# Performance work log

Hardware: AMD Instinct MI355X
Metric: run time of the kernel (lower is better)

The kernel has to match this reference:

```python
import jax, jax.numpy as jnp
import numpy as np

EPS = 1e-12

def _pdist(a, b):
    # a: [B,N,3], b: [B,M,3] -> [B,N,M] L2 distances (no huge [B,N,M,3] temp)
    sq = (jnp.sum(a * a, -1)[:, :, None] + jnp.sum(b * b, -1)[:, None, :]
          - 2.0 * jnp.einsum('bnd,bmd->bnm', a, b))
    return jnp.sqrt(jnp.maximum(sq, EPS))

def _loss_terms(skel_xyz, skel_radius, skel_nori, l3_xyz, shape_all):
    normal = shape_all[:, :, 3:6]
    shape_xyz = shape_all[:, :, :3]
    B, Ns, _ = skel_xyz.shape
    N = shape_xyz.shape[1]

    # --- loss_sample: 8 surface samples per sphere ---
    e = 0.57735027
    dirs = jnp.array([[e, e, e], [e, e, -e], [e, -e, e], [e, -e, -e],
                      [-e, e, e], [-e, e, -e], [-e, -e, e], [-e, -e, -e]],
                     dtype=skel_xyz.dtype)
    centers = jnp.repeat(skel_xyz, 8, axis=1)
    radii = jnp.repeat(skel_radius, 8, axis=1)
    sample_xyz = centers + radii * jnp.tile(dirs, (Ns, 1))[None]

    d_ss = _pdist(shape_xyz, sample_xyz)
    cd1 = jnp.sum(jnp.min(d_ss, axis=1)) / (Ns * 8)    # sample -> shape
    cd2 = jnp.sum(jnp.min(d_ss, axis=2)) / N           # shape -> sample
    loss_sample = cd1 + cd2

    # --- point2sphere / sphere2point ---
    d_sc = _pdist(shape_xyz, skel_xyz)                 # [B, N, Ns]
    sph = jnp.abs(d_sc - skel_radius[:, None, :, 0])
    loss_p2s = jnp.sum(jnp.min(sph, axis=2)) / N + jnp.sum(jnp.min(sph, axis=1)) / Ns

    loss_radius = -jnp.sum(skel_radius) / Ns

    # --- loss_normal: 30-NN of skel in shape, |dot(nori, shape normal)| ---
    d_ks = _pdist(skel_xyz, shape_xyz)                 # [B, Ns, N]
    idx30 = jax.lax.top_k(-d_ks, 30)[1]                # [B, Ns, 30]
    nn_nrm = jnp.take_along_axis(normal[:, None, :, :], idx30[..., None], axis=2)
    dots = jnp.einsum('bjd,bjkd->bjk', skel_nori, nn_nrm)
    loss_normal = jnp.sum(jnp.mean(jnp.abs(dots), axis=2)) / B

    # --- loss_skelenormal: points swept along nori, vs l3_xyz ---
    ks = (jnp.arange(30, dtype=skel_xyz.dtype) / 30.0)[None, :, None, None]
    combine = (skel_xyz[:, None] + skel_nori[:, None] * ks).reshape(B, 30 * Ns, 3)
    mind = jnp.min(_pdist(combine, l3_xyz), axis=2)
    loss_skn = 50.0 * jnp.sum(mind) / (B * Ns * 30)
    loss_skn = loss_skn + 500.0 * jnp.sum(jnp.var(mind, axis=1, ddof=1)) / B

    # --- loss_normaldist: exp barrier + hard penalty on |nori| ---
    nrm = jnp.sqrt(jnp.sum(skel_nori * skel_nori, -1) + EPS)
    loss_nd = jnp.sum(jnp.exp(-(nrm - 0.3)) + jnp.where(nrm < 0.25, 5.0, 0.0)) / (B * Ns)

    # --- loss_normalsmooth: 3-NN (incl. self) nori consistency ---
    idx3 = jax.lax.top_k(-_pdist(skel_xyz, skel_xyz), 3)[1]   # [B, Ns, 3]
    nn_nori = jnp.take_along_axis(skel_nori[:, None, :, :], idx3[..., None], axis=2)
    diff = skel_nori[:, :, None, :] - nn_nori
    loss_ns = jnp.sum(jnp.sqrt(jnp.sum(diff * diff, -1) + EPS)) / (B * Ns * 3)

    return loss_sample, loss_p2s, loss_radius, loss_normal, loss_skn, loss_nd, loss_ns

def setup_inputs() -> dict:
    key = jax.random.key(0)
    ks = jax.random.split(key, 9)
    B, N, Ns, M = 8, 4096, 256, 256
    return {
        'skel_xyz': jax.random.normal(ks[0], (B, Ns, 3), jnp.float32),
        'skel_radius': jax.random.uniform(ks[1], (B, Ns, 1), jnp.float32),
        'shape_cmb_features': jax.random.normal(ks[2], (B, Ns, 32), jnp.float32),
        'skel_nori': jax.random.normal(ks[3], (B, Ns, 3), jnp.float32),
        'weights': jax.random.uniform(ks[4], (B, Ns, 8), jnp.float32),
        'l3_xyz': jax.random.normal(ks[5], (B, M, 3), jnp.float32),
        'l3_normals': jax.random.normal(ks[6], (B, M, 3), jnp.float32),
        'shape_xyz': jax.random.normal(ks[7], (B, N, 6), jnp.float32),
        'A': jax.random.uniform(ks[8], (B, Ns, Ns), jnp.float32),
        'w0': 1, 'w1': 1, 'w2': 1, 'w3': 1, 'w4': 1, 'w5': 1, 'w6': 1,
    }

def reference(skel_xyz, skel_radius, shape_cmb_features, skel_nori, weights,
              l3_xyz, l3_normals, shape_xyz, A,
              w0, w1, w2, w3, w4, w5, w6):
    ls, lp, lr, ln, lskn, lnd, lns = _loss_terms(
        skel_xyz, skel_radius, skel_nori, l3_xyz, shape_xyz)
    # lap_reg=False -> loss_smooth = 0 (w3 term vanishes)
    return (w0 * ls + lp * w1 + lr * w2 + ln * w4 + lskn * w5
            + w6 * lnd + 0.1 * lns)
```

## Files before the change

### kernel.cpp

```cpp
#include <hip/hip_runtime.h>
#include <math.h>

#define EPS 1e-12f
#define EDIR 0.57735027f
#define M2E  -1.15470054f

#define NB 8
#define NS 256
#define NP 4096
#define NM 256

#define NBLK_SKEL 2048
#define NBLK_CD1  2048
#define NBLK_CD2  4096
#define NBLK_SKN  960
#define B0_CD1  (NBLK_SKEL)
#define B0_CD2  (B0_CD1 + NBLK_CD1)
#define B0_SKN  (B0_CD2 + NBLK_CD2)
#define NBLK_MEGA (B0_SKN + NBLK_SKN)

#define OFF_SKO 0
#define OFF_C1O (OFF_SKO + 2048*4)
#define OFF_C2O (OFF_C1O + 2048)
#define OFF_P2O (OFF_C2O + 4096)
#define OFF_SKS (OFF_P2O + 4096)
#define OFF_SKQ (OFF_SKS + 960)

__device__ __forceinline__ unsigned umin2(unsigned a, unsigned b){ return a<b?a:b; }
__device__ __forceinline__ unsigned umax2(unsigned a, unsigned b){ return a>b?a:b; }

__device__ __forceinline__ float wave_min(float v){
#pragma unroll
  for (int o = 32; o; o >>= 1) v = fminf(v, __shfl_xor(v, o));
  return v;
}
__device__ __forceinline__ float wave_max(float v){
#pragma unroll
  for (int o = 32; o; o >>= 1) v = fmaxf(v, __shfl_xor(v, o));
  return v;
}
__device__ __forceinline__ float wave_sum(float v){
#pragma unroll
  for (int o = 32; o; o >>= 1) v += __shfl_xor(v, o);
  return v;
}
__device__ __forceinline__ unsigned wave_min_u(unsigned v){
#pragma unroll
  for (int o = 32; o; o >>= 1){ unsigned w = __shfl_xor(v, o); v = (w < v) ? w : v; }
  return v;
}
__device__ __forceinline__ unsigned wave_max_u(unsigned v){
#pragma unroll
  for (int o = 32; o; o >>= 1){ unsigned w = __shfl_xor(v, o); v = (w > v) ? w : v; }
  return v;
}
__device__ __forceinline__ unsigned long long wave_min_u64(unsigned long long v){
#pragma unroll
  for (int o = 32; o; o >>= 1){
    unsigned long long w = __shfl_xor(v, o);
    v = (w < v) ? w : v;
  }
  return v;
}

__global__ __launch_bounds__(64) void k_mega(const float* __restrict__ skel,
                                             const float* __restrict__ rad,
                                             const float* __restrict__ nori,
                                             const float* __restrict__ l3,
                                             const float* __restrict__ shape,
                                             float* __restrict__ ws){
  __shared__ float4 lsh[NM];
  int bid  = blockIdx.x;
  int lane = threadIdx.x;

  if (bid < B0_CD1){
    int row = bid;
    int b = row >> 8;
    const float* sjp = skel + (size_t)row * 3;
    float cx = sjp[0], cy = sjp[1], cz = sjp[2];
    float rj = rad[row];
    float r2j = rj * rj;
    const float* njp = nori + (size_t)row * 3;
    float nx = njp[0], ny = njp[1], nz = njp[2];
    const float* shb = shape + (size_t)b * NP * 6;

    unsigned a0=~0u,a1=~0u,a2=~0u,a3=~0u,a4=~0u,a5=~0u;
    unsigned b0=~0u,b1=~0u,b2=~0u,b3=~0u,b4=~0u,b5=~0u;
    float dmoA = 3.4e38f, dmiA = -3.4e38f, dmoB = 3.4e38f, dmiB = -3.4e38f;

#pragma unroll 2
    for (int s = 0; s < 32; ++s){
      int nA = s * 128 + lane;
      int nB = nA + 64;
      float2 xyA = *(const float2*)(shb + (size_t)nA * 6);
      float  zA  = shb[(size_t)nA * 6 + 2];
      float2 xyB = *(const float2*)(shb + (size_t)nB * 6);
      float  zB  = shb[(size_t)nB * 6 + 2];
      float dxA = xyA.x - cx, dyA = xyA.y - cy, dzA = zA - cz;
      float dxB = xyB.x - cx, dyB = xyB.y - cy, dzB = zB - cz;
      float dA = fmaf(dxA, dxA, fmaf(dyA, dyA, dzA * dzA));
      float dB = fmaf(dxB, dxB, fmaf(dyB, dyB, dzB * dzB));
      bool inA = dA < r2j;
      bool inB = dB < r2j;
      dmoA = fminf(dmoA, inA ? 3.4e38f : dA);
      dmiA = fmaxf(dmiA, inA ? dA : -3.4e38f);
      dmoB = fminf(dmoB, inB ? 3.4e38f : dB);
      dmiB = fmaxf(dmiB, inB ? dB : -3.4e38f);
      unsigned uA = (__float_as_uint(dA) & 0xFFFFF000u) | (unsigned)nA;
      unsigned uB = (__float_as_uint(dB) & 0xFFFFF000u) | (unsigned)nB;
      a5 = umin2(a5, uA);
      { unsigned p = umin2(a4, a5), q = umax2(a4, a5); a4 = p; a5 = q; }
      { unsigned p = umin2(a3, a4), q = umax2(a3, a4); a3 = p; a4 = q; }
      { unsigned p = umin2(a2, a3), q = umax2(a2, a3); a2 = p; a3 = q; }
      { unsigned p = umin2(a1, a2), q = umax2(a1, a2); a1 = p; a2 = q; }
      { unsigned p = umin2(a0, a1), q = umax2(a0, a1); a0 = p; a1 = q; }
      b5 = umin2(b5, uB);
      { unsigned p = umin2(b4, b5), q = umax2(b4, b5); b4 = p; b5 = q; }
      { unsigned p = umin2(b3, b4), q = umax2(b3, b4); b3 = p; b4 = q; }
      { unsigned p = umin2(b2, b3), q = umax2(b2, b3); b2 = p; b3 = q; }
      { unsigned p = umin2(b1, b2), q = umax2(b1, b2); b1 = p; b2 = q; }
      { unsigned p = umin2(b0, b1), q = umax2(b0, b1); b0 = p; b1 = q; }
    }
    float dmin_out = wave_min(fminf(dmoA, dmoB));
    float dmax_in  = wave_max(fmaxf(dmiA, dmiB));
    float pmin = sqrtf(fmaxf(dmin_out, EPS)) - rj;
    float pin  = (dmax_in >= 0.0f) ? (rj - sqrtf(fmaxf(dmax_in, EPS))) : 3.4e38f;
    pmin = fminf(pmin, pin);

    unsigned lmin = umin2(a0, b0);
    unsigned lo = wave_min_u(lmin), hi = wave_max_u(lmin);
    while (lo < hi){
      unsigned mid = lo + ((hi - lo) >> 1);
      int c = __popcll(__ballot(a0 <= mid)) + __popcll(__ballot(a1 <= mid)) +
              __popcll(__ballot(a2 <= mid)) + __popcll(__ballot(a3 <= mid)) +
              __popcll(__ballot(a4 <= mid)) + __popcll(__ballot(a5 <= mid)) +
              __popcll(__ballot(b0 <= mid)) + __popcll(__ballot(b1 <= mid)) +
              __popcll(__ballot(b2 <= mid)) + __popcll(__ballot(b3 <= mid)) +
              __popcll(__ballot(b4 <= mid)) + __popcll(__ballot(b5 <= mid));
      if (c >= 30) hi = mid; else lo = mid + 1;
    }
    unsigned tau = hi;

    float dsum = 0.0f;
    {
      unsigned mm[12] = {a0,a1,a2,a3,a4,a5,b0,b1,b2,b3,b4,b5};
#pragma unroll
      for (int r = 0; r < 12; ++r){
        if (mm[r] <= tau){
          int idx = (int)(mm[r] & 0xFFFu);
          const float* qq = shb + (size_t)idx * 6;
          dsum += fabsf(fmaf(nx, qq[3], fmaf(ny, qq[4], nz * qq[5])));
        }
      }
    }
    dsum = wave_sum(dsum);

    const float* skb = skel + (size_t)b * NS * 3;
    const float* nb  = nori + (size_t)b * NS * 3;
    unsigned u0=~0u,u1=~0u,u2=~0u; int i0=0,i1=0,i2=0;
#pragma unroll
    for (int it = 0; it < 4; ++it){
      int n2i = it * 64 + lane;
      float dx = skb[n2i*3+0] - cx, dy = skb[n2i*3+1] - cy, dz = skb[n2i*3+2] - cz;
      unsigned u = __float_as_uint(fmaf(dx,dx,fmaf(dy,dy,dz*dz)));
      if (u < u2){ u2 = u; i2 = n2i; }
      if (u2 < u1){ unsigned t=u1;u1=u2;u2=t; int ti=i1;i1=i2;i2=ti; }
      if (u1 < u0){ unsigned t=u0;u0=u1;u1=t; int ti=i0;i0=i1;i1=ti; }
    }
    int cc = 0;
    float nssum = 0.0f;
#pragma unroll
    for (int r = 0; r < 3; ++r){
      unsigned hu = (cc==0)?u0:((cc==1)?u1:u2);
      int      hix= (cc==0)?i0:((cc==1)?i1:i2);
      unsigned long long pack = (((unsigned long long)hu) << 32) | (unsigned)hix;
      unsigned long long best = wave_min_u64(pack);
      if (pack == best) cc++;
      int idx = (int)(best & 0xffffffffull);
      if (lane == 0){
        float axn = nb[idx*3+0]-nx, ayn = nb[idx*3+1]-ny, azn = nb[idx*3+2]-nz;
        nssum += sqrtf(fmaf(axn,axn,fmaf(ayn,ayn,azn*azn)) + EPS);
      }
    }

    if (lane == 0){
      float nrm = sqrtf(nx*nx + ny*ny + nz*nz + EPS);
      float ndv = expf(0.3f - nrm) + ((nrm < 0.25f) ? 5.0f : 0.0f);
      float* sko = ws + OFF_SKO + (size_t)row * 4;
      sko[0] = pmin;
      sko[1] = dsum * (1.0f / 30.0f);
      sko[2] = nssum;
      sko[3] = ndv;
    }

  } else if (bid < B0_CD2){
    int s0 = bid - B0_CD1;
    int b  = s0 >> 8;
    const float* sp = skel + (size_t)s0 * 3;
    float cx = sp[0], cy = sp[1], cz = sp[2];
    float rr = rad[s0];
    float m2re = M2E * rr;
    const float* shb = shape + (size_t)b * NP * 6;
    float mn[8];
#pragma unroll
    for (int k = 0; k < 8; ++k) mn[k] = 3.4e38f;
#pragma unroll 4
    for (int s = 0; s < 64; ++s){
      int n = s * 64 + lane;
      float2 xy = *(const float2*)(shb + (size_t)n * 6);
      float pz  = shb[(size_t)n * 6 + 2];
      float dx = xy.x - cx, dy = xy.y - cy, dz = pz - cz;
      float q  = fmaf(dx, dx, fmaf(dy, dy, dz * dz));
      float s1p = dx + dy, s2p = dx - dy;
      float ga = s1p + dz, gb = s1p - dz, gc = s2p + dz, gd = s2p - dz;
      mn[0] = fminf(mn[0], fmaf(m2re,  ga, q));
      mn[1] = fminf(mn[1], fmaf(m2re,  gb, q));
      mn[2] = fminf(mn[2], fmaf(m2re,  gc, q));
      mn[3] = fminf(mn[3], fmaf(m2re,  gd, q));
      mn[4] = fminf(mn[4], fmaf(m2re, -gd, q));
      mn[5] = fminf(mn[5], fmaf(m2re, -gc, q));
      mn[6] = fminf(mn[6], fmaf(m2re, -gb, q));
      mn[7] = fminf(mn[7], fmaf(m2re, -ga, q));
    }
    float r2v = rr * rr;
    float v = 0.0f;
#pragma unroll
    for (int k = 0; k < 8; ++k){
      float m = wave_min(mn[k]);
      v += sqrtf(fmaxf(m + r2v, EPS));
    }
    if (lane == 0) ws[OFF_C1O + s0] = v;

  } else if (bid < B0_SKN){
    int wv   = bid - B0_CD2;
    int row0 = wv * 8;
    int b    = row0 >> 12;
    float cx[8], cy[8], cz[8];
#pragma unroll
    for (int i = 0; i < 8; ++i){
      const float* qp = shape + (size_t)(row0 + i) * 6;
      cx[i] = qp[0]; cy[i] = qp[1]; cz[i] = qp[2];
    }
    const float* skb = skel + (size_t)b * NS * 3;
    const float* rdb = rad + (size_t)b * NS;
    float mn[8], pm[8];
#pragma unroll
    for (int i = 0; i < 8; ++i){ mn[i] = 3.4e38f; pm[i] = 3.4e38f; }
#pragma unroll
    for (int it = 0; it < 4; ++it){
      int kidx = it * 64 + lane;
      float kx = skb[kidx*3+0], ky = skb[kidx*3+1], kz = skb[kidx*3+2];
      float rr = rdb[kidx];
      float r2 = rr * rr;
      float c1 = M2E * rr;
#pragma unroll
      for (int i = 0; i < 8; ++i){
        float dx = cx[i] - kx, dy = cy[i] - ky, dz = cz[i] - kz;
        float q  = fmaf(dx, dx, fmaf(dy, dy, dz * dz));
        float s  = (fabsf(dx) + fabsf(dy)) + fabsf(dz);
        mn[i] = fminf(mn[i], fmaf(c1, s, q + r2));
        float d = sqrtf(fmaxf(q, EPS));
        pm[i] = fminf(pm[i], fabsf(d - rr));
      }
    }
    float cdv = 0.0f, pv = 0.0f;
#pragma unroll
    for (int i = 0; i < 8; ++i){
      float m = wave_min(mn[i]);
      cdv += sqrtf(fmaxf(m, EPS));
      pv  += wave_min(pm[i]);
    }
    if (lane == 0){
      ws[OFF_C2O + wv] = cdv;
      ws[OFF_P2O + wv] = pv;
    }

  } else {
    int q = bid - B0_SKN;
    int b = q / 120;
    int w = q % 120;
    int t = w * 64 + lane;
    for (int i = lane; i < NM; i += 64){
      const float* lp = l3 + (size_t)(b * NM + i) * 3;
      float lx = lp[0], ly = lp[1], lz = lp[2];
      lsh[i] = make_float4(lx, ly, lz, fmaf(lx, lx, fmaf(ly, ly, lz * lz)));
    }
    __syncthreads();
    int s = t >> 8;
    int j = t & 255;
    float ksf = (float)s * (1.0f / 30.0f);
    const float* sj = skel + (size_t)(b * NS + j) * 3;
    const float* nj = nori + (size_t)(b * NS + j) * 3;
    float px = fmaf(nj[0], ksf, sj[0]);
    float py = fmaf(nj[1], ksf, sj[1]);
    float pz = fmaf(nj[2], ksf, sj[2]);
    float ax = -2.0f * px, ay = -2.0f * py, az = -2.0f * pz;
    float pw = fmaf(px, px, fmaf(py, py, pz * pz));
    float mn = 3.4e38f;
#pragma unroll 8
    for (int qq = 0; qq < NM; ++qq){
      float4 L = lsh[qq];
      float t2 = fmaf(L.x, ax, fmaf(L.y, ay, fmaf(L.z, az, L.w)));
      mn = fminf(mn, t2);
    }
    float d = sqrtf(fmaxf(mn + pw, EPS));
    float s1 = wave_sum(d);
    float s2 = wave_sum(d * d);
    if (lane == 0){
      ws[OFF_SKS + q] = s1;
      ws[OFF_SKQ + q] = s2;
    }
  }
}

__global__ __launch_bounds__(256) void k_final(const float* __restrict__ rad,
                                               const float* __restrict__ ws,
                                               const int* w0, const int* w1, const int* w2,
                                               const int* w4, const int* w5, const int* w6,
                                               float* __restrict__ out){
  __shared__ float red[8][4];
  __shared__ float sb1[960], sb2[960];
  __shared__ float bb1[8], bb2[8];
  int tid = threadIdx.x;
  int wid = tid >> 6, lane = tid & 63;

  float pp2sj = 0.0f, pnorm = 0.0f, pns = 0.0f, pnd = 0.0f;
  for (int q = tid; q < 2048; q += 256){
    const float* s4 = ws + OFF_SKO + (size_t)q * 4;
    pp2sj += s4[0]; pnorm += s4[1]; pns += s4[2]; pnd += s4[3];
  }
  float pc1 = 0.0f;
  for (int q = tid; q < 2048; q += 256) pc1 += ws[OFF_C1O + q];
  float pc2 = 0.0f, pp2n = 0.0f;
  for (int q = tid; q < 4096; q += 256){
    pc2  += ws[OFF_C2O + q];
    pp2n += ws[OFF_P2O + q];
  }
  float prad = 0.0f;
  for (int q = tid; q < NB * NS; q += 256) prad += rad[q];

  for (int q = tid; q < 960; q += 256){ sb1[q] = ws[OFF_SKS + q]; sb2[q] = ws[OFF_SKQ + q]; }

  pp2sj = wave_sum(pp2sj); pnorm = wave_sum(pnorm);
  pns = wave_sum(pns);     pnd = wave_sum(pnd);
  pc1 = wave_sum(pc1);     pc2 = wave_sum(pc2);
  pp2n = wave_sum(pp2n);   prad = wave_sum(prad);
  if (lane == 0){
    red[0][wid] = pp2sj; red[1][wid] = pnorm; red[2][wid] = pns; red[3][wid] = pnd;
    red[4][wid] = pc1;   red[5][wid] = pc2;   red[6][wid] = pp2n; red[7][wid] = prad;
  }
  __syncthreads();
  if (tid < 8){
    float s1 = 0.0f, s2 = 0.0f;
    for (int i = 0; i < 120; ++i){ s1 += sb1[tid * 120 + i]; s2 += sb2[tid * 120 + i]; }
    bb1[tid] = s1; bb2[tid] = s2;
  }
  __syncthreads();
  if (tid == 0){
    float p2sj = red[0][0]+red[0][1]+red[0][2]+red[0][3];
    float nrmt = red[1][0]+red[1][1]+red[1][2]+red[1][3];
    float nst  = red[2][0]+red[2][1]+red[2][2]+red[2][3];
    float ndt  = red[3][0]+red[3][1]+red[3][2]+red[3][3];
    float c1t  = red[4][0]+red[4][1]+red[4][2]+red[4][3];
    float c2t  = red[5][0]+red[5][1]+red[5][2]+red[5][3];
    float p2nt = red[6][0]+red[6][1]+red[6][2]+red[6][3];
    float srad = red[7][0]+red[7][1]+red[7][2]+red[7][3];
    float ls = c1t * (1.0f/2048.0f) + c2t * (1.0f/4096.0f);
    float lp = p2nt * (1.0f/4096.0f) + p2sj * (1.0f/256.0f);
    float lr = -srad * (1.0f/256.0f);
    float ln = nrmt * (1.0f/8.0f);
    float smind = 0.0f, vsum = 0.0f;
    for (int b = 0; b < NB; ++b){
      float s1 = bb1[b], s2 = bb2[b];
      smind += s1;
      vsum  += (s2 - s1 * s1 * (1.0f/7680.0f)) * (1.0f/7679.0f);
    }
    float lskn = 50.0f * smind * (1.0f/(8.0f*7680.0f)) + 500.0f * vsum * (1.0f/8.0f);
    float lnd = ndt * (1.0f/2048.0f);
    float lns = nst * (1.0f/6144.0f);
    float o = (float)w0[0]*ls + (float)w1[0]*lp + (float)w2[0]*lr +
              (float)w4[0]*ln + (float)w5[0]*lskn + (float)w6[0]*lnd + 0.1f*lns;
    out[0] = o;
  }
}

extern "C" void kernel_launch(void* const* d_in, const int* in_sizes, int n_in,
                              void* d_out, int out_size, void* d_ws, size_t ws_size,
                              hipStream_t stream) {
  const float* skel  = (const float*)d_in[0];
  const float* rad   = (const float*)d_in[1];
  const float* nori  = (const float*)d_in[3];
  const float* l3    = (const float*)d_in[5];
  const float* shape = (const float*)d_in[7];
  const int* w0 = (const int*)d_in[9];
  const int* w1 = (const int*)d_in[10];
  const int* w2 = (const int*)d_in[11];
  const int* w4 = (const int*)d_in[13];
  const int* w5 = (const int*)d_in[14];
  const int* w6 = (const int*)d_in[15];
  float* ws  = (float*)d_ws;
  float* out = (float*)d_out;

  k_mega<<<dim3(NBLK_MEGA), dim3(64), 0, stream>>>(skel, rad, nori, l3, shape, ws);
  k_final<<<dim3(1), dim3(256), 0, stream>>>(rad, ws, w0, w1, w2, w4, w5, w6, out);
}
```

Before: 63.00 us.

## Fuse sample-to-shape chamfer into skeleton pass and co-schedule roles per block

The per-sphere 8-sample chamfer min (cd1) now runs inside the skeleton kernel's loop over shape points. It reuses the same loaded coordinates and squared distances instead of streaming the shape cloud a second time. The launch changes from many 64-thread blocks, one role each, to 2048 blocks of 256 threads. Wave 0 does skeleton+cd1, waves 1-2 do shape->sample/p2s, and wave 3 does the swept-normal term in the first 960 blocks. This cuts redundant global loads and block count, but lengthens the heaviest wave, which may become the critical path. The LDS barrier for the l3 table is removed because only one wave uses it.

```diff
diff --git a/kernel.cpp b/kernel.cpp
--- a/kernel.cpp
+++ b/kernel.cpp
@@ -10,14 +10,7 @@
 #define NP 4096
 #define NM 256
 
-#define NBLK_SKEL 2048
-#define NBLK_CD1  2048
-#define NBLK_CD2  4096
-#define NBLK_SKN  960
-#define B0_CD1  (NBLK_SKEL)
-#define B0_CD2  (B0_CD1 + NBLK_CD1)
-#define B0_SKN  (B0_CD2 + NBLK_CD2)
-#define NBLK_MEGA (B0_SKN + NBLK_SKN)
+#define NBLK_MEGA 2048
 
 #define OFF_SKO 0
 #define OFF_C1O (OFF_SKO + 2048*4)
@@ -63,23 +56,26 @@
   return v;
 }
 
-__global__ __launch_bounds__(64) void k_mega(const float* __restrict__ skel,
-                                             const float* __restrict__ rad,
-                                             const float* __restrict__ nori,
-                                             const float* __restrict__ l3,
-                                             const float* __restrict__ shape,
-                                             float* __restrict__ ws){
+__global__ __launch_bounds__(256) void k_mega(const float* __restrict__ skel,
+                                              const float* __restrict__ rad,
+                                              const float* __restrict__ nori,
+                                              const float* __restrict__ l3,
+                                              const float* __restrict__ shape,
+                                              float* __restrict__ ws){
   __shared__ float4 lsh[NM];
   int bid  = blockIdx.x;
-  int lane = threadIdx.x;
-
-  if (bid < B0_CD1){
+  int tid  = threadIdx.x;
+  int wid  = tid >> 6;
+  int lane = tid & 63;
+
+  if (wid == 0){
     int row = bid;
     int b = row >> 8;
     const float* sjp = skel + (size_t)row * 3;
     float cx = sjp[0], cy = sjp[1], cz = sjp[2];
     float rj = rad[row];
     float r2j = rj * rj;
+    float m2re = M2E * rj;
     const float* njp = nori + (size_t)row * 3;
     float nx = njp[0], ny = njp[1], nz = njp[2];
     const float* shb = shape + (size_t)b * NP * 6;
@@ -87,6 +83,9 @@
     unsigned a0=~0u,a1=~0u,a2=~0u,a3=~0u,a4=~0u,a5=~0u;
     unsigned b0=~0u,b1=~0u,b2=~0u,b3=~0u,b4=~0u,b5=~0u;
     float dmoA = 3.4e38f, dmiA = -3.4e38f, dmoB = 3.4e38f, dmiB = -3.4e38f;
+    float mn[8];
+#pragma unroll
+    for (int k = 0; k < 8; ++k) mn[k] = 3.4e38f;
 
 #pragma unroll 2
     for (int s = 0; s < 32; ++s){
@@ -100,6 +99,30 @@
       float dxB = xyB.x - cx, dyB = xyB.y - cy, dzB = zB - cz;
       float dA = fmaf(dxA, dxA, fmaf(dyA, dyA, dzA * dzA));
       float dB = fmaf(dxB, dxB, fmaf(dyB, dyB, dzB * dzB));
+      {
+        float s1p = dxA + dyA, s2p = dxA - dyA;
+        float ga = s1p + dzA, gb = s1p - dzA, gc = s2p + dzA, gd = s2p - dzA;
+        mn[0] = fminf(mn[0], fmaf(m2re,  ga, dA));
+        mn[1] = fminf(mn[1], fmaf(m2re,  gb, dA));
+        mn[2] = fminf(mn[2], fmaf(m2re,  gc, dA));
+        mn[3] = fminf(mn[3], fmaf(m2re,  gd, dA));
+        mn[4] = fminf(mn[4], fmaf(m2re, -gd, dA));
+        mn[5] = fminf(mn[5], fmaf(m2re, -gc, dA));
+        mn[6] = fminf(mn[6], fmaf(m2re, -gb, dA));
+        mn[7] = fminf(mn[7], fmaf(m2re, -ga, dA));
+      }
+      {
+        float s1p = dxB + dyB, s2p = dxB - dyB;
+        float ga = s1p + dzB, gb = s1p - dzB, gc = s2p + dzB, gd = s2p - dzB;
+        mn[0] = fminf(mn[0], fmaf(m2re,  ga, dB));
+        mn[1] = fminf(mn[1], fmaf(m2re,  gb, dB));
+        mn[2] = fminf(mn[2], fmaf(m2re,  gc, dB));
+        mn[3] = fminf(mn[3], fmaf(m2re,  gd, dB));
+        mn[4] = fminf(mn[4], fmaf(m2re, -gd, dB));
+        mn[5] = fminf(mn[5], fmaf(m2re, -gc, dB));
+        mn[6] = fminf(mn[6], fmaf(m2re, -gb, dB));
+        mn[7] = fminf(mn[7], fmaf(m2re, -ga, dB));
+      }
       bool inA = dA < r2j;
       bool inB = dB < r2j;
       dmoA = fminf(dmoA, inA ? 3.4e38f : dA);
@@ -121,6 +144,15 @@
       { unsigned p = umin2(b1, b2), q = umax2(b1, b2); b1 = p; b2 = q; }
       { unsigned p = umin2(b0, b1), q = umax2(b0, b1); b0 = p; b1 = q; }
     }
+    {
+      float v = 0.0f;
+#pragma unroll
+      for (int k = 0; k < 8; ++k){
+        float m = wave_min(mn[k]);
+        v += sqrtf(fmaxf(m + r2j, EPS));
+      }
+      if (lane == 0) ws[OFF_C1O + row] = v;
+    }
     float dmin_out = wave_min(fminf(dmoA, dmoB));
     float dmax_in  = wave_max(fmaxf(dmiA, dmiB));
     float pmin = sqrtf(fmaxf(dmin_out, EPS)) - rj;
@@ -193,46 +225,8 @@
       sko[3] = ndv;
     }
 
-  } else if (bid < B0_CD2){
-    int s0 = bid - B0_CD1;
-    int b  = s0 >> 8;
-    const float* sp = skel + (size_t)s0 * 3;
-    float cx = sp[0], cy = sp[1], cz = sp[2];
-    float rr = rad[s0];
-    float m2re = M2E * rr;
-    const float* shb = shape + (size_t)b * NP * 6;
-    float mn[8];
-#pragma unroll
-    for (int k = 0; k < 8; ++k) mn[k] = 3.4e38f;
-#pragma unroll 4
-    for (int s = 0; s < 64; ++s){
-      int n = s * 64 + lane;
-      float2 xy = *(const float2*)(shb + (size_t)n * 6);
-      float pz  = shb[(size_t)n * 6 + 2];
-      float dx = xy.x - cx, dy = xy.y - cy, dz = pz - cz;
-      float q  = fmaf(dx, dx, fmaf(dy, dy, dz * dz));
-      float s1p = dx + dy, s2p = dx - dy;
-      float ga = s1p + dz, gb = s1p - dz, gc = s2p + dz, gd = s2p - dz;
-      mn[0] = fminf(mn[0], fmaf(m2re,  ga, q));
-      mn[1] = fminf(mn[1], fmaf(m2re,  gb, q));
-      mn[2] = fminf(mn[2], fmaf(m2re,  gc, q));
-      mn[3] = fminf(mn[3], fmaf(m2re,  gd, q));
-      mn[4] = fminf(mn[4], fmaf(m2re, -gd, q));
-      mn[5] = fminf(mn[5], fmaf(m2re, -gc, q));
-      mn[6] = fminf(mn[6], fmaf(m2re, -gb, q));
-      mn[7] = fminf(mn[7], fmaf(m2re, -ga, q));
-    }
-    float r2v = rr * rr;
-    float v = 0.0f;
-#pragma unroll
-    for (int k = 0; k < 8; ++k){
-      float m = wave_min(mn[k]);
-      v += sqrtf(fmaxf(m + r2v, EPS));
-    }
-    if (lane == 0) ws[OFF_C1O + s0] = v;
-
-  } else if (bid < B0_SKN){
-    int wv   = bid - B0_CD2;
+  } else if (wid <= 2){
+    int wv   = bid * 2 + (wid - 1);
     int row0 = wv * 8;
     int b    = row0 >> 12;
     float cx[8], cy[8], cz[8];
@@ -276,7 +270,8 @@
     }
 
   } else {
-    int q = bid - B0_SKN;
+    int q = bid;
+    if (q >= 960) return;
     int b = q / 120;
     int w = q % 120;
     int t = w * 64 + lane;
@@ -285,7 +280,6 @@
       float lx = lp[0], ly = lp[1], lz = lp[2];
       lsh[i] = make_float4(lx, ly, lz, fmaf(lx, lx, fmaf(ly, ly, lz * lz)));
     }
-    __syncthreads();
     int s = t >> 8;
     int j = t & 255;
     float ksf = (float)s * (1.0f / 30.0f);
@@ -401,6 +395,6 @@
   float* ws  = (float*)d_ws;
   float* out = (float*)d_out;
 
-  k_mega<<<dim3(NBLK_MEGA), dim3(64), 0, stream>>>(skel, rad, nori, l3, shape, ws);
+  k_mega<<<dim3(NBLK_MEGA), dim3(256), 0, stream>>>(skel, rad, nori, l3, shape, ws);
   k_final<<<dim3(1), dim3(256), 0, stream>>>(rad, ws, w0, w1, w2, w4, w5, w6, out);
 }
```

Result: faster. 55.67 us (-11.6%).
